# Optimization experiments

Hardware: AMD Instinct MI355X
Metric: run time of the kernel (lower is better)

The kernel has to match this reference:

```python
import jax, jax.numpy as jnp
import numpy as np

IN_DIM, HID_DIM, OUT_DIM, N_EXP = 3, 20, 3, 5
BATCH = 1 << 20


def setup_inputs() -> dict:
    key = jax.random.key(0)
    ks = jax.random.split(key, 8)
    s_in = 1.0 / np.sqrt(IN_DIM)
    s_hid = 1.0 / np.sqrt(HID_DIM)
    return {
        "x": jax.random.normal(ks[0], (BATCH, IN_DIM), dtype=jnp.float32),
        # stacked expert params: fc1 [E, in, hid], fc2 [E, hid, out]
        "W1": jax.random.uniform(ks[1], (N_EXP, IN_DIM, HID_DIM), jnp.float32, -s_in, s_in),
        "b1": jax.random.uniform(ks[2], (N_EXP, HID_DIM), jnp.float32, -s_in, s_in),
        "W2": jax.random.uniform(ks[3], (N_EXP, HID_DIM, OUT_DIM), jnp.float32, -s_hid, s_hid),
        "b2": jax.random.uniform(ks[4], (N_EXP, OUT_DIM), jnp.float32, -s_hid, s_hid),
        # gate Linear(in, n_experts)
        "Wg": jax.random.uniform(ks[5], (IN_DIM, N_EXP), jnp.float32, -s_in, s_in),
        "bg": jax.random.uniform(ks[6], (N_EXP,), jnp.float32, -s_in, s_in),
    }


def reference(x, W1, b1, W2, b2, Wg, bg):
    # all experts as one batched GEMM: h [B, E, hid]
    h = jax.nn.relu(jnp.einsum("bi,eih->beh", x, W1) + b1)
    expert_out = jnp.einsum("beh,eho->beo", h, W2) + b2  # [B, E, out]
    gate = jax.nn.softmax(x @ Wg + bg, axis=-1)           # [B, E]
    mixed = jnp.einsum("be,beo->bo", gate, expert_out)    # [B, out]
    return (mixed, gate)
```

## Files before the change

kernel.cpp:

```cpp
#include <hip/hip_runtime.h>

#define IN_DIM  3
#define HID_DIM 20
#define OUT_DIM 3
#define N_EXP   5
#define ELEMS   4
#define PAIRS   (ELEMS / 2)
#define BLOCK   256
#define SPAN    (BLOCK * ELEMS)


typedef float v2f __attribute__((ext_vector_type(2)));

__global__ __launch_bounds__(BLOCK) void moe_kernel(
    const float* __restrict__ x,
    const float* __restrict__ W1,
    const float* __restrict__ b1,
    const float* __restrict__ W2,
    const float* __restrict__ b2,
    const float* __restrict__ Wg,
    const float* __restrict__ bg,
    float* __restrict__ out,
    int B)
{
    __shared__ float4 sW[N_EXP * HID_DIM * 2];
    __shared__ float  sIO[SPAN * N_EXP];

    const int t = threadIdx.x;

    if (t < N_EXP * HID_DIM) {
        const int e = t / HID_DIM, j = t % HID_DIM;
        float4 a, w;
        a.x = W1[(e * IN_DIM + 0) * HID_DIM + j];
        a.y = W1[(e * IN_DIM + 1) * HID_DIM + j];
        a.z = W1[(e * IN_DIM + 2) * HID_DIM + j];
        a.w = b1[e * HID_DIM + j];
        w.x = W2[(e * HID_DIM + j) * OUT_DIM + 0];
        w.y = W2[(e * HID_DIM + j) * OUT_DIM + 1];
        w.z = W2[(e * HID_DIM + j) * OUT_DIM + 2];
        w.w = 0.f;
        sW[2 * t]     = a;
        sW[2 * t + 1] = w;
    }

    const long long blockBase = (long long)blockIdx.x * SPAN;
    float* __restrict__ mixed_out = out;
    float* __restrict__ gate_out  = out + (long long)B * OUT_DIM;

    if (blockBase + SPAN <= (long long)B) {
        const size_t bb = (size_t)blockBase;

        {
            const float4* g4 = reinterpret_cast<const float4*>(x + bb * IN_DIM);
            float4* s4 = reinterpret_cast<float4*>(sIO);
            #pragma unroll
            for (int k = 0; k < 3; ++k) s4[t + k * BLOCK] = g4[t + k * BLOCK];
        }
        __syncthreads();

        v2f xp[PAIRS][IN_DIM];
        {
            const float4* s4 = reinterpret_cast<const float4*>(sIO);
            float xf[ELEMS * IN_DIM];
            #pragma unroll
            for (int k = 0; k < 3; ++k) {
                float4 v = s4[3 * t + k];
                xf[4 * k + 0] = v.x; xf[4 * k + 1] = v.y;
                xf[4 * k + 2] = v.z; xf[4 * k + 3] = v.w;
            }
            #pragma unroll
            for (int p = 0; p < PAIRS; ++p)
                #pragma unroll
                for (int i = 0; i < IN_DIM; ++i)
                    xp[p][i] = (v2f){xf[(2 * p) * IN_DIM + i],
                                     xf[(2 * p + 1) * IN_DIM + i]};
        }
        __syncthreads();

        v2f gatep[PAIRS][N_EXP];
        #pragma unroll
        for (int p = 0; p < PAIRS; ++p) {
            v2f lg[N_EXP];
            #pragma unroll
            for (int e = 0; e < N_EXP; ++e) {
                v2f v = (v2f){bg[e], bg[e]};
                #pragma unroll
                for (int i = 0; i < IN_DIM; ++i) {
                    const float w = Wg[i * N_EXP + e];
                    v = __builtin_elementwise_fma(xp[p][i], (v2f){w, w}, v);
                }
                lg[e] = (v2f){__expf(v.x), __expf(v.y)};
            }
            v2f s = (v2f){0.f, 0.f};
            #pragma unroll
            for (int e = 0; e < N_EXP; ++e) s += lg[e];
            const v2f inv = (v2f){1.0f / s.x, 1.0f / s.y};
            #pragma unroll
            for (int e = 0; e < N_EXP; ++e) gatep[p][e] = lg[e] * inv;
        }
        {
            float4* s4 = reinterpret_cast<float4*>(sIO);
            float g[ELEMS * N_EXP];
            #pragma unroll
            for (int p = 0; p < PAIRS; ++p)
                #pragma unroll
                for (int e = 0; e < N_EXP; ++e) {
                    g[(2 * p) * N_EXP + e]     = gatep[p][e].x;
                    g[(2 * p + 1) * N_EXP + e] = gatep[p][e].y;
                }
            #pragma unroll
            for (int k = 0; k < 5; ++k)
                s4[5 * t + k] = make_float4(g[4 * k + 0], g[4 * k + 1],
                                            g[4 * k + 2], g[4 * k + 3]);
        }
        __syncthreads();

        {
            float4* o4 = reinterpret_cast<float4*>(gate_out + bb * N_EXP);
            const float4* s4 = reinterpret_cast<const float4*>(sIO);
            #pragma unroll
            for (int k = 0; k < 5; ++k) o4[t + k * BLOCK] = s4[t + k * BLOCK];
        }

        v2f mix[PAIRS][OUT_DIM];
        #pragma unroll
        for (int p = 0; p < PAIRS; ++p)
            #pragma unroll
            for (int k = 0; k < OUT_DIM; ++k) mix[p][k] = (v2f){0.f, 0.f};

        #pragma unroll
        for (int e = 0; e < N_EXP; ++e) {
            v2f oacc[PAIRS][OUT_DIM];
            #pragma unroll
            for (int p = 0; p < PAIRS; ++p)
                #pragma unroll
                for (int k = 0; k < OUT_DIM; ++k) {
                    const float bk = b2[e * OUT_DIM + k];
                    oacc[p][k] = (v2f){bk, bk};
                }
            #pragma unroll
            for (int j = 0; j < HID_DIM; ++j) {
                const float4 a = sW[(e * HID_DIM + j) * 2];
                const float4 w = sW[(e * HID_DIM + j) * 2 + 1];
                const v2f w10v = (v2f){a.x, a.x}, w11v = (v2f){a.y, a.y};
                const v2f w12v = (v2f){a.z, a.z}, bb1v = (v2f){a.w, a.w};
                const v2f w20v = (v2f){w.x, w.x}, w21v = (v2f){w.y, w.y};
                const v2f w22v = (v2f){w.z, w.z};
                #pragma unroll
                for (int p = 0; p < PAIRS; ++p) {
                    v2f h = __builtin_elementwise_fma(xp[p][2], w12v,
                            __builtin_elementwise_fma(xp[p][1], w11v,
                            __builtin_elementwise_fma(xp[p][0], w10v, bb1v)));
                    h = __builtin_elementwise_max(h, (v2f){0.f, 0.f});
                    oacc[p][0] = __builtin_elementwise_fma(h, w20v, oacc[p][0]);
                    oacc[p][1] = __builtin_elementwise_fma(h, w21v, oacc[p][1]);
                    oacc[p][2] = __builtin_elementwise_fma(h, w22v, oacc[p][2]);
                }
            }
            #pragma unroll
            for (int p = 0; p < PAIRS; ++p)
                #pragma unroll
                for (int k = 0; k < OUT_DIM; ++k)
                    mix[p][k] = __builtin_elementwise_fma(gatep[p][e], oacc[p][k],
                                                          mix[p][k]);
        }
        __syncthreads();

        {
            float4* s4 = reinterpret_cast<float4*>(sIO);
            float m[ELEMS * OUT_DIM];
            #pragma unroll
            for (int p = 0; p < PAIRS; ++p)
                #pragma unroll
                for (int k = 0; k < OUT_DIM; ++k) {
                    m[(2 * p) * OUT_DIM + k]     = mix[p][k].x;
                    m[(2 * p + 1) * OUT_DIM + k] = mix[p][k].y;
                }
            #pragma unroll
            for (int k = 0; k < 3; ++k)
                s4[3 * t + k] = make_float4(m[4 * k + 0], m[4 * k + 1],
                                            m[4 * k + 2], m[4 * k + 3]);
        }
        __syncthreads();

        {
            float4* o4 = reinterpret_cast<float4*>(mixed_out + bb * OUT_DIM);
            const float4* s4 = reinterpret_cast<const float4*>(sIO);
            #pragma unroll
            for (int k = 0; k < 3; ++k) o4[t + k * BLOCK] = s4[t + k * BLOCK];
        }
    } else {
        __syncthreads();
        for (int c = 0; c < ELEMS; ++c) {
            const long long bidx = blockBase + (long long)c * BLOCK + t;
            if (bidx >= (long long)B) continue;
            float xv[IN_DIM];
            for (int i = 0; i < IN_DIM; ++i) xv[i] = x[bidx * IN_DIM + i];

            float lg[N_EXP]; float s = 0.f;
            for (int e = 0; e < N_EXP; ++e) {
                float v = bg[e];
                for (int i = 0; i < IN_DIM; ++i)
                    v = fmaf(xv[i], Wg[i * N_EXP + e], v);
                v = __expf(v); lg[e] = v; s += v;
            }
            const float inv = 1.0f / s;
            for (int e = 0; e < N_EXP; ++e) lg[e] *= inv;

            float mixv[OUT_DIM] = {0.f, 0.f, 0.f};
            for (int e = 0; e < N_EXP; ++e) {
                for (int k = 0; k < OUT_DIM; ++k)
                    mixv[k] = fmaf(lg[e], b2[e * OUT_DIM + k], mixv[k]);
                for (int j = 0; j < HID_DIM; ++j) {
                    const float4 a = sW[(e * HID_DIM + j) * 2];
                    const float4 w = sW[(e * HID_DIM + j) * 2 + 1];
                    float h = fmaf(xv[2], a.z, fmaf(xv[1], a.y, fmaf(xv[0], a.x, a.w)));
                    h = fmaxf(h, 0.f);
                    const float hg = h * lg[e];
                    mixv[0] = fmaf(hg, w.x, mixv[0]);
                    mixv[1] = fmaf(hg, w.y, mixv[1]);
                    mixv[2] = fmaf(hg, w.z, mixv[2]);
                }
            }
            for (int k = 0; k < OUT_DIM; ++k)
                mixed_out[bidx * OUT_DIM + k] = mixv[k];
            for (int e = 0; e < N_EXP; ++e)
                gate_out[bidx * N_EXP + e] = lg[e];
        }
    }
}

extern "C" void kernel_launch(void* const* d_in, const int* in_sizes, int n_in,
                              void* d_out, int out_size, void* d_ws, size_t ws_size,
                              hipStream_t stream) {
    const float* x  = (const float*)d_in[0];
    const float* W1 = (const float*)d_in[1];
    const float* b1 = (const float*)d_in[2];
    const float* W2 = (const float*)d_in[3];
    const float* b2 = (const float*)d_in[4];
    const float* Wg = (const float*)d_in[5];
    const float* bg = (const float*)d_in[6];
    float* out = (float*)d_out;

    const int B = in_sizes[0] / IN_DIM;
    const int grid = (B + SPAN - 1) / SPAN;

    moe_kernel<<<grid, BLOCK, 0, stream>>>(x, W1, b1, W2, b2, Wg, bg, out, B);
}
```

Before: 108.6 us.

## Drop shared-memory IO staging; load and store rows directly with float2

Removes the shared-memory staging buffer for x, gate and mixed outputs. Each thread now reads and writes its four contiguous rows directly with float2 accesses. This cuts several block barriers and the LDS round trips, and shrinks LDS use, which should raise occupancy. In exchange, global accesses become strided per thread (48-80 byte stride) rather than fully coalesced float4, and the hidden loop is only partially unrolled by 2. The tail path is also reordered to match the main path's arithmetic.

Result: no change. 110.3 us (+1.6%).

```diff
diff --git a/kernel.cpp b/kernel.cpp
--- a/kernel.cpp
+++ b/kernel.cpp
@@ -5,7 +5,7 @@
 #define OUT_DIM 3
 #define N_EXP   5
 #define ELEMS   4
-#define PAIRS   (ELEMS / 2)
+#define PAIRS   2
 #define BLOCK   256
 #define SPAN    (BLOCK * ELEMS)
 
@@ -24,7 +24,6 @@
     int B)
 {
     __shared__ float4 sW[N_EXP * HID_DIM * 2];
-    __shared__ float  sIO[SPAN * N_EXP];
 
     const int t = threadIdx.x;
 
@@ -42,45 +41,33 @@
         sW[2 * t]     = a;
         sW[2 * t + 1] = w;
     }
-
-    const long long blockBase = (long long)blockIdx.x * SPAN;
+    __syncthreads();
+
+    const long long g = (long long)blockIdx.x * BLOCK + t;
+    const long long base = 4 * g;
     float* __restrict__ mixed_out = out;
     float* __restrict__ gate_out  = out + (long long)B * OUT_DIM;
 
-    if (blockBase + SPAN <= (long long)B) {
-        const size_t bb = (size_t)blockBase;
-
-        {
-            const float4* g4 = reinterpret_cast<const float4*>(x + bb * IN_DIM);
-            float4* s4 = reinterpret_cast<float4*>(sIO);
-            #pragma unroll
-            for (int k = 0; k < 3; ++k) s4[t + k * BLOCK] = g4[t + k * BLOCK];
-        }
-        __syncthreads();
-
+    if (base + ELEMS <= (long long)B) {
         v2f xp[PAIRS][IN_DIM];
         {
-            const float4* s4 = reinterpret_cast<const float4*>(sIO);
-            float xf[ELEMS * IN_DIM];
-            #pragma unroll
-            for (int k = 0; k < 3; ++k) {
-                float4 v = s4[3 * t + k];
-                xf[4 * k + 0] = v.x; xf[4 * k + 1] = v.y;
-                xf[4 * k + 2] = v.z; xf[4 * k + 3] = v.w;
-            }
-            #pragma unroll
-            for (int p = 0; p < PAIRS; ++p)
-                #pragma unroll
-                for (int i = 0; i < IN_DIM; ++i)
-                    xp[p][i] = (v2f){xf[(2 * p) * IN_DIM + i],
-                                     xf[(2 * p + 1) * IN_DIM + i]};
-        }
-        __syncthreads();
+            const float2* x2 = reinterpret_cast<const float2*>(x + 3 * base);
+            #pragma unroll
+            for (int p = 0; p < PAIRS; ++p) {
+                float2 a = x2[3 * p + 0];
+                float2 b = x2[3 * p + 1];
+                float2 c = x2[3 * p + 2];
+                xp[p][0] = (v2f){a.x, b.y};
+                xp[p][1] = (v2f){a.y, c.x};
+                xp[p][2] = (v2f){b.x, c.y};
+            }
+        }
 
         v2f gatep[PAIRS][N_EXP];
         #pragma unroll
         for (int p = 0; p < PAIRS; ++p) {
             v2f lg[N_EXP];
+            v2f s = (v2f){0.f, 0.f};
             #pragma unroll
             for (int e = 0; e < N_EXP; ++e) {
                 v2f v = (v2f){bg[e], bg[e]};
@@ -90,36 +77,23 @@
                     v = __builtin_elementwise_fma(xp[p][i], (v2f){w, w}, v);
                 }
                 lg[e] = (v2f){__expf(v.x), __expf(v.y)};
-            }
-            v2f s = (v2f){0.f, 0.f};
-            #pragma unroll
-            for (int e = 0; e < N_EXP; ++e) s += lg[e];
+                s += lg[e];
+            }
             const v2f inv = (v2f){1.0f / s.x, 1.0f / s.y};
             #pragma unroll
             for (int e = 0; e < N_EXP; ++e) gatep[p][e] = lg[e] * inv;
         }
+
         {
-            float4* s4 = reinterpret_cast<float4*>(sIO);
-            float g[ELEMS * N_EXP];
-            #pragma unroll
-            for (int p = 0; p < PAIRS; ++p)
-                #pragma unroll
-                for (int e = 0; e < N_EXP; ++e) {
-                    g[(2 * p) * N_EXP + e]     = gatep[p][e].x;
-                    g[(2 * p + 1) * N_EXP + e] = gatep[p][e].y;
-                }
-            #pragma unroll
-            for (int k = 0; k < 5; ++k)
-                s4[5 * t + k] = make_float4(g[4 * k + 0], g[4 * k + 1],
-                                            g[4 * k + 2], g[4 * k + 3]);
-        }
-        __syncthreads();
-
-        {
-            float4* o4 = reinterpret_cast<float4*>(gate_out + bb * N_EXP);
-            const float4* s4 = reinterpret_cast<const float4*>(sIO);
-            #pragma unroll
-            for (int k = 0; k < 5; ++k) o4[t + k * BLOCK] = s4[t + k * BLOCK];
+            float2* g2 = reinterpret_cast<float2*>(gate_out + 5 * base);
+            #pragma unroll
+            for (int p = 0; p < PAIRS; ++p) {
+                g2[5 * p + 0] = make_float2(gatep[p][0].x, gatep[p][1].x);
+                g2[5 * p + 1] = make_float2(gatep[p][2].x, gatep[p][3].x);
+                g2[5 * p + 2] = make_float2(gatep[p][4].x, gatep[p][0].y);
+                g2[5 * p + 3] = make_float2(gatep[p][1].y, gatep[p][2].y);
+                g2[5 * p + 4] = make_float2(gatep[p][3].y, gatep[p][4].y);
+            }
         }
 
         v2f mix[PAIRS][OUT_DIM];
@@ -138,23 +112,20 @@
                     const float bk = b2[e * OUT_DIM + k];
                     oacc[p][k] = (v2f){bk, bk};
                 }
-            #pragma unroll
+            #pragma unroll 2
             for (int j = 0; j < HID_DIM; ++j) {
                 const float4 a = sW[(e * HID_DIM + j) * 2];
                 const float4 w = sW[(e * HID_DIM + j) * 2 + 1];
-                const v2f w10v = (v2f){a.x, a.x}, w11v = (v2f){a.y, a.y};
-                const v2f w12v = (v2f){a.z, a.z}, bb1v = (v2f){a.w, a.w};
-                const v2f w20v = (v2f){w.x, w.x}, w21v = (v2f){w.y, w.y};
-                const v2f w22v = (v2f){w.z, w.z};
                 #pragma unroll
                 for (int p = 0; p < PAIRS; ++p) {
-                    v2f h = __builtin_elementwise_fma(xp[p][2], w12v,
-                            __builtin_elementwise_fma(xp[p][1], w11v,
-                            __builtin_elementwise_fma(xp[p][0], w10v, bb1v)));
+                    v2f h = __builtin_elementwise_fma(xp[p][2], (v2f){a.z, a.z},
+                            __builtin_elementwise_fma(xp[p][1], (v2f){a.y, a.y},
+                            __builtin_elementwise_fma(xp[p][0], (v2f){a.x, a.x},
+                                                      (v2f){a.w, a.w})));
                     h = __builtin_elementwise_max(h, (v2f){0.f, 0.f});
-                    oacc[p][0] = __builtin_elementwise_fma(h, w20v, oacc[p][0]);
-                    oacc[p][1] = __builtin_elementwise_fma(h, w21v, oacc[p][1]);
-                    oacc[p][2] = __builtin_elementwise_fma(h, w22v, oacc[p][2]);
+                    oacc[p][0] = __builtin_elementwise_fma(h, (v2f){w.x, w.x}, oacc[p][0]);
+                    oacc[p][1] = __builtin_elementwise_fma(h, (v2f){w.y, w.y}, oacc[p][1]);
+                    oacc[p][2] = __builtin_elementwise_fma(h, (v2f){w.z, w.z}, oacc[p][2]);
                 }
             }
             #pragma unroll
@@ -164,36 +135,20 @@
                     mix[p][k] = __builtin_elementwise_fma(gatep[p][e], oacc[p][k],
                                                           mix[p][k]);
         }
-        __syncthreads();
 
         {
-            float4* s4 = reinterpret_cast<float4*>(sIO);
-            float m[ELEMS * OUT_DIM];
-            #pragma unroll
-            for (int p = 0; p < PAIRS; ++p)
-                #pragma unroll
-                for (int k = 0; k < OUT_DIM; ++k) {
-                    m[(2 * p) * OUT_DIM + k]     = mix[p][k].x;
-                    m[(2 * p + 1) * OUT_DIM + k] = mix[p][k].y;
-                }
-            #pragma unroll
-            for (int k = 0; k < 3; ++k)
-                s4[3 * t + k] = make_float4(m[4 * k + 0], m[4 * k + 1],
-                                            m[4 * k + 2], m[4 * k + 3]);
-        }
-        __syncthreads();
-
-        {
-            float4* o4 = reinterpret_cast<float4*>(mixed_out + bb * OUT_DIM);
-            const float4* s4 = reinterpret_cast<const float4*>(sIO);
-            #pragma unroll
-            for (int k = 0; k < 3; ++k) o4[t + k * BLOCK] = s4[t + k * BLOCK];
+            float2* m2 = reinterpret_cast<float2*>(mixed_out + 3 * base);
+            #pragma unroll
+            for (int p = 0; p < PAIRS; ++p) {
+                m2[3 * p + 0] = make_float2(mix[p][0].x, mix[p][1].x);
+                m2[3 * p + 1] = make_float2(mix[p][2].x, mix[p][0].y);
+                m2[3 * p + 2] = make_float2(mix[p][1].y, mix[p][2].y);
+            }
         }
     } else {
-        __syncthreads();
         for (int c = 0; c < ELEMS; ++c) {
-            const long long bidx = blockBase + (long long)c * BLOCK + t;
-            if (bidx >= (long long)B) continue;
+            const long long bidx = base + c;
+            if (bidx >= (long long)B) break;
             float xv[IN_DIM];
             for (int i = 0; i < IN_DIM; ++i) xv[i] = x[bidx * IN_DIM + i];
 
@@ -209,18 +164,19 @@
 
             float mixv[OUT_DIM] = {0.f, 0.f, 0.f};
             for (int e = 0; e < N_EXP; ++e) {
-                for (int k = 0; k < OUT_DIM; ++k)
-                    mixv[k] = fmaf(lg[e], b2[e * OUT_DIM + k], mixv[k]);
+                float oa[OUT_DIM];
+                for (int k = 0; k < OUT_DIM; ++k) oa[k] = b2[e * OUT_DIM + k];
                 for (int j = 0; j < HID_DIM; ++j) {
                     const float4 a = sW[(e * HID_DIM + j) * 2];
                     const float4 w = sW[(e * HID_DIM + j) * 2 + 1];
                     float h = fmaf(xv[2], a.z, fmaf(xv[1], a.y, fmaf(xv[0], a.x, a.w)));
                     h = fmaxf(h, 0.f);
-                    const float hg = h * lg[e];
-                    mixv[0] = fmaf(hg, w.x, mixv[0]);
-                    mixv[1] = fmaf(hg, w.y, mixv[1]);
-                    mixv[2] = fmaf(hg, w.z, mixv[2]);
-                }
+                    oa[0] = fmaf(h, w.x, oa[0]);
+                    oa[1] = fmaf(h, w.y, oa[1]);
+                    oa[2] = fmaf(h, w.z, oa[2]);
+                }
+                for (int k = 0; k < OUT_DIM; ++k)
+                    mixv[k] = fmaf(lg[e], oa[k], mixv[k]);
             }
             for (int k = 0; k < OUT_DIM; ++k)
                 mixed_out[bidx * OUT_DIM + k] = mixv[k];
```
